# Kernel optimization log

Measured on AMD Instinct MI355X. Metric: run time of the kernel, lower is better.

Reference implementation:

```python
import jax, jax.numpy as jnp
import numpy as np

PATCH = 3
ALPHA = 0.1

def unfold_patches(f, p):
    # Emulates F.unfold with zero padding p//2, stride 1: [B,C,H,W] -> [B, C*p*p, H, W].
    # Descriptor-dim ordering differs from torch's, but the correlation sum over the
    # descriptor dim is permutation-invariant, so the output is identical.
    pad = p // 2
    B, C, H, W = f.shape
    fp = jnp.pad(f, ((0, 0), (0, 0), (pad, pad), (pad, pad)))
    patches = [fp[:, :, i:i + H, j:j + W] for i in range(p) for j in range(p)]
    return jnp.concatenate(patches, axis=1)


def setup_inputs() -> dict:
    key = jax.random.key(0)
    k1, k2 = jax.random.split(key)
    x_rgb = jax.random.uniform(k1, (4, 3, 64, 64), dtype=jnp.float32)
    feature = jax.random.normal(k2, (4, 64, 64, 64), dtype=jnp.float32)
    return {"x_rgb": x_rgb, "feature": feature}


def reference(x_rgb, feature):
    B, _, H, W = x_rgb.shape
    HW = H * W
    rgb = x_rgb.reshape(B, 3, HW).transpose(0, 2, 1)            # [B, HW, 3]
    local = unfold_patches(feature, PATCH).reshape(B, -1, HW)    # [B, D, HW], D = C*p*p
    # correlation = K^T K over descriptor dim -> [B, HW, HW]
    corr = jnp.einsum('bdp,bdq->bpq', local, local)
    attn = jax.nn.softmax(corr / ALPHA, axis=-1)
    weighted = jnp.einsum('bpq,bqc->bpc', attn, rgb)             # [B, HW, 3]
    return weighted.transpose(0, 2, 1).reshape(B, 3, H, W)
```

## Files before the change

kernel.cpp:

```cpp
#include <hip/hip_runtime.h>
#include <hip/hip_bf16.h>

typedef __attribute__((ext_vector_type(4))) float f32x4;
typedef __attribute__((ext_vector_type(2))) long long l64x2;

constexpr int kB = 4, kC = 64, kH = 64, kW = 64;
constexpr int kHW = kH * kW;
constexpr int kD  = kC * 9;
constexpr int KSPLIT = 8;
constexpr int KBLK = 16;
constexpr int QWAVE = 32;
constexpr int QWG = 128;
constexpr int NTILE = kHW / KSPLIT / KBLK;
constexpr int ROWB8 = 640;
constexpr int TILEB = KBLK * ROWB8;
constexpr int TCHUNK = TILEB / 16;

#define FSCALE 3.79828370f
#define FS2    14.4269504089f
#define SEED_SLACK 64.0f

__global__ __launch_bounds__(256)
void nlwa_selfsq(const float* __restrict__ feat, float* __restrict__ sq) {
    int idx = blockIdx.x * 256 + threadIdx.x;
    if (idx >= kB * kHW) return;
    int b = idx >> 12, p = idx & 4095;
    const float* f = feat + (size_t)b * kC * kHW + p;
    float s = 0.f;
    #pragma unroll 8
    for (int c = 0; c < kC; ++c) { float v = f[c * kHW]; s = fmaf(v, v, s); }
    sq[idx] = s;
}

__global__ __launch_bounds__(256)
void nlwa_unfold(const float* __restrict__ feat, unsigned char* __restrict__ Kd) {
    int idx = blockIdx.x * 256 + threadIdx.x;
    if (idx >= kB * kHW * kD) return;
    int d = idx % kD;
    int v = (idx / kD) % kHW;
    int b = idx / (kD * kHW);
    int c = d / 9, dl = d % 9;
    int y = (v >> 6) + dl / 3 - 1;
    int x = (v & 63) + dl % 3 - 1;
    float val = 0.f;
    if ((unsigned)y < 64u && (unsigned)x < 64u)
        val = feat[((b * kC + c) * kH + y) * kW + x] * FSCALE;
    unsigned int fb = __builtin_bit_cast(unsigned int, val * 0x1p-120f);
    unsigned int mag = ((fb & 0x7fffffffu) + 0x80000u) >> 20;
    if (mag > 0x7eu) mag = 0x7eu;
    unsigned char u8 = (unsigned char)(((fb >> 31) << 7) | mag);
    int w = d >> 5, kg = (d >> 3) & 3, e = d & 7;
    int cp = ((w >> 1) * 4 + kg) ^ (v & 7);
    Kd[(size_t)(b * kHW + v) * ROWB8 + cp * 16 + (w & 1) * 8 + e] = u8;
}

__global__ __launch_bounds__(256, 4)
void nlwa_attn(const unsigned char* __restrict__ Kd,
               const float* __restrict__ rgb,
               const float* __restrict__ sq,
               float* __restrict__ part) {
    __shared__ alignas(16) unsigned char Ks[2][KBLK][ROWB8];

    int orig = blockIdx.x;
    int wg = (orig & 7) * 128 + (orig >> 3);
    int qblk = wg & 31;
    int pr = wg >> 5;
    int ks = pr & 7;
    int b  = pr >> 3;

    int tid = threadIdx.x, lane = tid & 63, wid = tid >> 6;
    int lr = lane & 15, lg = lane >> 4;
    int x7 = lr & 7;
    int qwave = qblk * QWG + wid * QWAVE;
    int k0 = ks * (kHW / KSPLIT);

    int4 qb[2][9];
    #pragma unroll
    for (int g = 0; g < 2; ++g) {
        const unsigned char* qbase = Kd + (size_t)(b * kHW + qwave + g * 16 + lr) * ROWB8;
        #pragma unroll
        for (int p = 0; p < 9; ++p)
            qb[g][p] = *(const int4*)(qbase + (((p * 4 + lg) ^ x7) << 4));
    }

    float m[2], l[2] = {0.f, 0.f};
    float O[2][3] = {{0,0,0},{0,0,0}};
    const float* sqb = sq + b * kHW;
    #pragma unroll
    for (int g = 0; g < 2; ++g) {
        int q = qwave + g * 16 + lr, y = q >> 6, x = q & 63;
        float s = 0.f;
        #pragma unroll
        for (int dy = -1; dy <= 1; ++dy)
            #pragma unroll
            for (int dx = -1; dx <= 1; ++dx) {
                int yy = y + dy, xx = x + dx;
                if ((unsigned)yy < 64u && (unsigned)xx < 64u) s += sqb[yy * 64 + xx];
            }
        m[g] = s * FS2 - SEED_SLACK;
    }

    const unsigned char* ksrc = Kd + (size_t)(b * kHW + k0) * ROWB8;
    unsigned char* lds0 = &Ks[0][0][0];

    auto stage = [&](int t, int bufi) {
        const unsigned char* src = ksrc + (size_t)t * TILEB;
        unsigned char* dstb = lds0 + bufi * TILEB;
        #pragma unroll
        for (int it = 0; it < 3; ++it) {
            int base = it * 256 + wid * 64;
            if (base < TCHUNK) {
                __builtin_amdgcn_global_load_lds(
                    (const __attribute__((address_space(1))) void*)(src + (size_t)(base + lane) * 16),
                    (__attribute__((address_space(3))) void*)(dstb + (size_t)base * 16),
                    16, 0, 0);
            }
        }
    };

    stage(0, 0);
    __syncthreads();

    int lo2 = x7 & 3, h = x7 >> 2;
    int r0 = lr * ROWB8 + ((lg ^ lo2) << 4);
    int e0 = r0 + h * 64, o0 = r0 - h * 64;

    int buf = 0;
    for (int t = 0; t < NTILE; ++t) {
        if (t + 1 < NTILE) stage(t + 1, buf ^ 1);

        const unsigned char* kb = lds0 + buf * TILEB;
        f32x4 acc[2];
        acc[0] = (f32x4){0.f, 0.f, 0.f, 0.f};
        acc[1] = (f32x4){0.f, 0.f, 0.f, 0.f};

        #pragma unroll
        for (int p = 0; p < 9; ++p) {
            int4 ka = *(const int4*)(kb + ((p & 1) ? o0 : e0) + p * 64);
            l64x2 ka64 = __builtin_bit_cast(l64x2, ka);
            #pragma unroll
            for (int w01 = 0; w01 < 2; ++w01) {
                long long a0 = ka64[w01];
                #pragma unroll
                for (int g = 0; g < 2; ++g) {
                    long long bq = __builtin_bit_cast(l64x2, qb[g][p])[w01];
                    acc[g] = __builtin_amdgcn_mfma_f32_16x16x32_fp8_fp8(a0, bq, acc[g], 0, 0, 0);
                }
            }
        }

        float pm[2];
        #pragma unroll
        for (int g = 0; g < 2; ++g)
            pm[g] = fmaxf(fmaxf(acc[g][0], acc[g][1]), fmaxf(acc[g][2], acc[g][3]));

        float dmx = fmaxf(pm[0] - m[0], pm[1] - m[1]);
        if (__any(dmx >= -25.f)) {
            int kt0 = k0 + t * KBLK;
            #pragma unroll
            for (int g = 0; g < 2; ++g) {
                float v = pm[g];
                v = fmaxf(v, __shfl_xor(v, 16));
                v = fmaxf(v, __shfl_xor(v, 32));
                float mn = fmaxf(m[g], v);
                float al = exp2f(m[g] - mn);
                m[g] = mn;
                l[g] *= al;
                O[g][0] *= al; O[g][1] *= al; O[g][2] *= al;
            }
            float4 rv[3];
            #pragma unroll
            for (int c = 0; c < 3; ++c)
                rv[c] = *(const float4*)(rgb + (size_t)(b * 3 + c) * kHW + kt0 + lg * 4);
            #pragma unroll
            for (int g = 0; g < 2; ++g) {
                float p0 = exp2f(acc[g][0] - m[g]);
                float p1 = exp2f(acc[g][1] - m[g]);
                float p2 = exp2f(acc[g][2] - m[g]);
                float p3 = exp2f(acc[g][3] - m[g]);
                l[g] += p0 + p1 + p2 + p3;
                #pragma unroll
                for (int c = 0; c < 3; ++c)
                    O[g][c] += p0 * rv[c].x + p1 * rv[c].y + p2 * rv[c].z + p3 * rv[c].w;
            }
        }
        __syncthreads();
        buf ^= 1;
    }

    #pragma unroll
    for (int g = 0; g < 2; ++g) {
        l[g] += __shfl_xor(l[g], 16); l[g] += __shfl_xor(l[g], 32);
        #pragma unroll
        for (int c = 0; c < 3; ++c) {
            O[g][c] += __shfl_xor(O[g][c], 16);
            O[g][c] += __shfl_xor(O[g][c], 32);
        }
    }
    if (lg == 0) {
        #pragma unroll
        for (int g = 0; g < 2; ++g) {
            int q = qwave + g * 16 + lr;
            float* p = part + ((size_t)(b * kHW + q) * KSPLIT + ks) * 5;
            p[0] = m[g]; p[1] = l[g]; p[2] = O[g][0]; p[3] = O[g][1]; p[4] = O[g][2];
        }
    }
}

__global__ __launch_bounds__(256)
void nlwa_merge(const float* __restrict__ part, float* __restrict__ out) {
    int idx = blockIdx.x * 256 + threadIdx.x;
    if (idx >= kB * kHW) return;
    int b = idx >> 12, q = idx & 4095;
    const float* p = part + (size_t)idx * KSPLIT * 5;
    float M = -INFINITY;
    #pragma unroll
    for (int s = 0; s < KSPLIT; ++s) M = fmaxf(M, p[s * 5]);
    float L = 0.f, o0 = 0.f, o1 = 0.f, o2 = 0.f;
    #pragma unroll
    for (int s = 0; s < KSPLIT; ++s) {
        float a = exp2f(p[s * 5] - M);
        L  += p[s * 5 + 1] * a;
        o0 += p[s * 5 + 2] * a;
        o1 += p[s * 5 + 3] * a;
        o2 += p[s * 5 + 4] * a;
    }
    float inv = 1.f / L;
    out[(b * 3 + 0) * kHW + q] = o0 * inv;
    out[(b * 3 + 1) * kHW + q] = o1 * inv;
    out[(b * 3 + 2) * kHW + q] = o2 * inv;
}

__global__ __launch_bounds__(64)
void nlwa_naive(const float* __restrict__ feat, const float* __restrict__ rgb,
                float* __restrict__ out) {
    int p = blockIdx.x, b = blockIdx.y;
    int pi = p >> 6, pj = p & 63;
    int t = threadIdx.x;
    __shared__ float pdesc[kD];
    __shared__ float rows[kC][3][kW];
    __shared__ float red[64][5];

    for (int d = t; d < kD; d += 64) {
        int c = d / 9, dl = d % 9;
        int y = pi + dl / 3 - 1, x = pj + dl % 3 - 1;
        pdesc[d] = ((unsigned)y < 64u && (unsigned)x < 64u)
                 ? feat[((b * kC + c) * kH + y) * kW + x] : 0.f;
    }
    float m = -INFINITY, l = 0.f, O0 = 0.f, O1 = 0.f, O2 = 0.f;
    for (int qi = 0; qi < kH; ++qi) {
        __syncthreads();
        for (int f = t; f < kC * 3 * kW; f += 64) {
            int x = f & 63, yy = (f >> 6) % 3, c = f / (3 * kW);
            int y = qi + yy - 1;
            rows[c][yy][x] = ((unsigned)y < 64u) ? feat[((b * kC + c) * kH + y) * kW + x] : 0.f;
        }
        __syncthreads();
        float s = 0.f;
        for (int c = 0; c < kC; ++c)
            for (int dl = 0; dl < 9; ++dl) {
                int x = t + dl % 3 - 1;
                float fv = ((unsigned)x < 64u) ? rows[c][dl / 3][x] : 0.f;
                s += pdesc[c * 9 + dl] * fv;
            }
        s *= 14.4269504089f;
        int q = qi * 64 + t;
        float mn = fmaxf(m, s);
        float al = exp2f(m - mn);
        float pv = exp2f(s - mn);
        l = l * al + pv;
        O0 = O0 * al + pv * rgb[(b * 3 + 0) * kHW + q];
        O1 = O1 * al + pv * rgb[(b * 3 + 1) * kHW + q];
        O2 = O2 * al + pv * rgb[(b * 3 + 2) * kHW + q];
        m = mn;
    }
    red[t][0] = m; red[t][1] = l; red[t][2] = O0; red[t][3] = O1; red[t][4] = O2;
    __syncthreads();
    if (t == 0) {
        float M = -INFINITY;
        for (int i = 0; i < 64; ++i) M = fmaxf(M, red[i][0]);
        float L = 0, A = 0, Bv = 0, Cv = 0;
        for (int i = 0; i < 64; ++i) {
            float a = exp2f(red[i][0] - M);
            L += red[i][1] * a; A += red[i][2] * a; Bv += red[i][3] * a; Cv += red[i][4] * a;
        }
        out[(b * 3 + 0) * kHW + p] = A / L;
        out[(b * 3 + 1) * kHW + p] = Bv / L;
        out[(b * 3 + 2) * kHW + p] = Cv / L;
    }
}

extern "C" void kernel_launch(void* const* d_in, const int* in_sizes, int n_in,
                              void* d_out, int out_size, void* d_ws, size_t ws_size,
                              hipStream_t stream) {
    const float* x_rgb   = (const float*)d_in[0];
    const float* feature = (const float*)d_in[1];
    float* out = (float*)d_out;

    size_t needK = (size_t)kB * kHW * ROWB8;
    size_t needP = (size_t)kB * kHW * KSPLIT * 5 * 4;
    size_t needS = (size_t)kB * kHW * 4;
    if (ws_size >= needK + needP + needS) {
        unsigned char* Kd = (unsigned char*)d_ws;
        float* partb = (float*)((char*)d_ws + needK);
        float* sqb   = (float*)((char*)d_ws + needK + needP);
        int total = kB * kHW * kD;
        nlwa_selfsq<<<(kB * kHW + 255) / 256, 256, 0, stream>>>(feature, sqb);
        nlwa_unfold<<<(total + 255) / 256, 256, 0, stream>>>(feature, Kd);
        nlwa_attn<<<kB * (kHW / QWG) * KSPLIT, 256, 0, stream>>>(Kd, x_rgb, sqb, partb);
        nlwa_merge<<<(kB * kHW + 255) / 256, 256, 0, stream>>>(partb, out);
    } else {
        nlwa_naive<<<dim3(kHW, kB), 64, 0, stream>>>(feature, x_rgb, out);
    }
}
```

Measured before the change: 89.58 us.

## Switch QK to scaled 16x16x128 fp8 MFMA and pack unfold writes

Replaces the 16x16x32 fp8 MFMA chain (18 instructions per tile per group) with 5 scaled 16x16x128 f8f6f4 MFMAs using unit scales. The K row layout changes to 128-byte groups with an XOR swizzle so that 32-byte operands can be loaded as two 16-byte LDS reads. Padding out to 640 bytes (zeros in the last 64) adds some wasted MAC work. The unfold kernel now has each thread pack and write 8 bytes instead of single bytes, which cuts the number of threads and stores.

New measurement: 97.66 us. 9.0% more time.

```diff
diff --git a/kernel.cpp b/kernel.cpp
--- a/kernel.cpp
+++ b/kernel.cpp
@@ -2,7 +2,7 @@
 #include <hip/hip_bf16.h>
 
 typedef __attribute__((ext_vector_type(4))) float f32x4;
-typedef __attribute__((ext_vector_type(2))) long long l64x2;
+typedef __attribute__((ext_vector_type(8))) int i32x8;
 
 constexpr int kB = 4, kC = 64, kH = 64, kW = 64;
 constexpr int kHW = kH * kW;
@@ -19,6 +19,7 @@
 #define FSCALE 3.79828370f
 #define FS2    14.4269504089f
 #define SEED_SLACK 64.0f
+#define SCL1 0x7F7F7F7F
 
 __global__ __launch_bounds__(256)
 void nlwa_selfsq(const float* __restrict__ feat, float* __restrict__ sq) {
@@ -35,23 +36,32 @@
 __global__ __launch_bounds__(256)
 void nlwa_unfold(const float* __restrict__ feat, unsigned char* __restrict__ Kd) {
     int idx = blockIdx.x * 256 + threadIdx.x;
-    if (idx >= kB * kHW * kD) return;
-    int d = idx % kD;
-    int v = (idx / kD) % kHW;
-    int b = idx / (kD * kHW);
-    int c = d / 9, dl = d % 9;
-    int y = (v >> 6) + dl / 3 - 1;
-    int x = (v & 63) + dl % 3 - 1;
-    float val = 0.f;
-    if ((unsigned)y < 64u && (unsigned)x < 64u)
-        val = feat[((b * kC + c) * kH + y) * kW + x] * FSCALE;
-    unsigned int fb = __builtin_bit_cast(unsigned int, val * 0x1p-120f);
-    unsigned int mag = ((fb & 0x7fffffffu) + 0x80000u) >> 20;
-    if (mag > 0x7eu) mag = 0x7eu;
-    unsigned char u8 = (unsigned char)(((fb >> 31) << 7) | mag);
-    int w = d >> 5, kg = (d >> 3) & 3, e = d & 7;
-    int cp = ((w >> 1) * 4 + kg) ^ (v & 7);
-    Kd[(size_t)(b * kHW + v) * ROWB8 + cp * 16 + (w & 1) * 8 + e] = u8;
+    if (idx >= kB * kHW * (ROWB8 / 8)) return;
+    int piece = idx % (ROWB8 / 8);
+    int v = (idx / (ROWB8 / 8)) % kHW;
+    int b = idx / ((ROWB8 / 8) * kHW);
+    unsigned long long pack = 0ULL;
+    if (piece < 72) {
+        int y0 = v >> 6, x0 = v & 63;
+        #pragma unroll
+        for (int j = 0; j < 8; ++j) {
+            int d = piece * 8 + j;
+            int c = d / 9, dl = d % 9;
+            int y = y0 + dl / 3 - 1;
+            int x = x0 + dl % 3 - 1;
+            float val = 0.f;
+            if ((unsigned)y < 64u && (unsigned)x < 64u)
+                val = feat[((b * kC + c) * kH + y) * kW + x] * FSCALE;
+            unsigned int fb = __builtin_bit_cast(unsigned int, val * 0x1p-120f);
+            unsigned int mag = ((fb & 0x7fffffffu) + 0x80000u) >> 20;
+            if (mag > 0x7eu) mag = 0x7eu;
+            unsigned long long u8 = ((fb >> 31) << 7) | mag;
+            pack |= u8 << (8 * j);
+        }
+    }
+    int c16 = piece >> 1, half = piece & 1;
+    int cp = c16 ^ (v & 7);
+    *(unsigned long long*)(Kd + (size_t)(b * kHW + v) * ROWB8 + cp * 16 + half * 8) = pack;
 }
 
 __global__ __launch_bounds__(256, 4)
@@ -70,17 +80,22 @@
 
     int tid = threadIdx.x, lane = tid & 63, wid = tid >> 6;
     int lr = lane & 15, lg = lane >> 4;
-    int x7 = lr & 7;
+    int s7 = lr & 7;
     int qwave = qblk * QWG + wid * QWAVE;
     int k0 = ks * (kHW / KSPLIT);
 
-    int4 qb[2][9];
+    i32x8 qb[2][5];
     #pragma unroll
     for (int g = 0; g < 2; ++g) {
-        const unsigned char* qbase = Kd + (size_t)(b * kHW + qwave + g * 16 + lr) * ROWB8;
-        #pragma unroll
-        for (int p = 0; p < 9; ++p)
-            qb[g][p] = *(const int4*)(qbase + (((p * 4 + lg) ^ x7) << 4));
+        int qrow = qwave + g * 16 + lr;
+        const unsigned char* qbase = Kd + (size_t)(b * kHW + qrow) * ROWB8;
+        int sq7 = qrow & 7;
+        #pragma unroll
+        for (int W = 0; W < 5; ++W) {
+            int4 lo = *(const int4*)(qbase + W * 128 + (((lg * 2)     ^ sq7) << 4));
+            int4 hi = *(const int4*)(qbase + W * 128 + (((lg * 2 + 1) ^ sq7) << 4));
+            qb[g][W] = (i32x8){lo.x, lo.y, lo.z, lo.w, hi.x, hi.y, hi.z, hi.w};
+        }
     }
 
     float m[2], l[2] = {0.f, 0.f};
@@ -121,9 +136,8 @@
     stage(0, 0);
     __syncthreads();
 
-    int lo2 = x7 & 3, h = x7 >> 2;
-    int r0 = lr * ROWB8 + ((lg ^ lo2) << 4);
-    int e0 = r0 + h * 64, o0 = r0 - h * 64;
+    int eA = lr * ROWB8 + (((lg * 2)     ^ s7) << 4);
+    int eB = lr * ROWB8 + (((lg * 2 + 1) ^ s7) << 4);
 
     int buf = 0;
     for (int t = 0; t < NTILE; ++t) {
@@ -135,18 +149,14 @@
         acc[1] = (f32x4){0.f, 0.f, 0.f, 0.f};
 
         #pragma unroll
-        for (int p = 0; p < 9; ++p) {
-            int4 ka = *(const int4*)(kb + ((p & 1) ? o0 : e0) + p * 64);
-            l64x2 ka64 = __builtin_bit_cast(l64x2, ka);
-            #pragma unroll
-            for (int w01 = 0; w01 < 2; ++w01) {
-                long long a0 = ka64[w01];
-                #pragma unroll
-                for (int g = 0; g < 2; ++g) {
-                    long long bq = __builtin_bit_cast(l64x2, qb[g][p])[w01];
-                    acc[g] = __builtin_amdgcn_mfma_f32_16x16x32_fp8_fp8(a0, bq, acc[g], 0, 0, 0);
-                }
-            }
+        for (int W = 0; W < 5; ++W) {
+            int4 lo = *(const int4*)(kb + eA + W * 128);
+            int4 hi = *(const int4*)(kb + eB + W * 128);
+            i32x8 a = (i32x8){lo.x, lo.y, lo.z, lo.w, hi.x, hi.y, hi.z, hi.w};
+            acc[0] = __builtin_amdgcn_mfma_scale_f32_16x16x128_f8f6f4(
+                        a, qb[0][W], acc[0], 0, 0, 0, SCL1, 0, SCL1);
+            acc[1] = __builtin_amdgcn_mfma_scale_f32_16x16x128_f8f6f4(
+                        a, qb[1][W], acc[1], 0, 0, 0, SCL1, 0, SCL1);
         }
 
         float pm[2];
@@ -304,9 +314,9 @@
         unsigned char* Kd = (unsigned char*)d_ws;
         float* partb = (float*)((char*)d_ws + needK);
         float* sqb   = (float*)((char*)d_ws + needK + needP);
-        int total = kB * kHW * kD;
+        int pieces = kB * kHW * (ROWB8 / 8);
         nlwa_selfsq<<<(kB * kHW + 255) / 256, 256, 0, stream>>>(feature, sqb);
-        nlwa_unfold<<<(total + 255) / 256, 256, 0, stream>>>(feature, Kd);
+        nlwa_unfold<<<(pieces + 255) / 256, 256, 0, stream>>>(feature, Kd);
         nlwa_attn<<<kB * (kHW / QWG) * KSPLIT, 256, 0, stream>>>(Kd, x_rgb, sqb, partb);
         nlwa_merge<<<(kB * kHW + 255) / 256, 256, 0, stream>>>(partb, out);
     } else {
```
